# Kernel optimization log

Measured on AMD Instinct MI355X. Metric: run time of the kernel, lower is better.

The kernel has to match this reference:

```python
import jax, jax.numpy as jnp
import numpy as np

B, D_IN, H, D_OUT = 256, 512, 512, 10
S = 32          # num posterior samples
MAXITER = 10    # fixed CG steps (solve_normaleq_cg_fixed_step_reortho(maxiter=10))
EPS = 1e-12


def mlp(params, x):
    W1, b1, W2, b2 = params
    h = jnp.tanh(x @ W1 + b1)
    return h @ W2 + b2  # [B, D_OUT]


def setup_inputs() -> dict:
    key = jax.random.key(0)
    ks = jax.random.split(key, 8)
    s = lambda k, shape, scale=1.0: jax.random.normal(k, shape, dtype=jnp.float32) * scale
    return {
        "x": s(ks[0], (B, D_IN)),
        "W1": s(ks[1], (D_IN, H), 1.0 / np.sqrt(D_IN)),
        "b1": jnp.zeros((H,), jnp.float32),
        "W2": s(ks[2], (H, D_OUT), 1.0 / np.sqrt(H)),
        "b2": jnp.zeros((D_OUT,), jnp.float32),
        "eps_W1": s(ks[3], (S, D_IN, H)),
        "eps_b1": s(ks[4], (S, H)),
        "eps_W2": s(ks[5], (S, H, D_OUT)),
        "eps_b2": s(ks[6], (S, D_OUT)),
        "log_precision": jnp.zeros((), jnp.float32),
        "log_scale_image": jnp.asarray(-2.0, jnp.float32),
    }


def _posterior_predict(x, W1, b1, W2, b2, eps_W1, eps_b1, eps_W2, eps_b2,
                       log_precision, log_scale_image):
    params = (W1, b1, W2, b2)
    f = lambda p: mlp(p, x)
    out0, jvp_lin = jax.linearize(f, params)  # out0: [B, D_OUT]
    _, vjp_fn = jax.vjp(f, params)
    N = B * D_OUT

    def matvec(u_flat):  # u: [N] -> (J J^T) u : [N]
        (t,) = vjp_fn(u_flat.reshape(B, D_OUT))  # J^T u (param pytree)
        return jvp_lin(t).ravel()                # J J^T u

    def cg_reortho(b):  # fixed-step CG with full reorthogonalization
        rn0 = jnp.linalg.norm(b)
        basis0 = jnp.zeros((MAXITER + 1, N), b.dtype).at[0].set(b / (rn0 + EPS))

        def step(carry, k):
            a, r, p, basis = carry
            Ap = matvec(p)
            rr = jnp.vdot(r, r)
            alpha = rr / (jnp.vdot(p, Ap) + EPS)
            a = a + alpha * p
            r_new = r - alpha * Ap
            # Gram-Schmidt reorthogonalization against stored residual basis
            r_new = r_new - basis.T @ (basis @ r_new)
            beta = jnp.vdot(r_new, r_new) / (rr + EPS)
            p = r_new + beta * p
            basis = basis.at[k + 1].set(r_new / (jnp.linalg.norm(r_new) + EPS))
            return (a, r_new, p, basis), jnp.linalg.norm(r_new)

        init = (jnp.zeros_like(b), b, b, basis0)
        (a, _, _, _), resnorms = jax.lax.scan(step, init, jnp.arange(MAXITER))
        return a, resnorms

    def kernel_projection(eps):  # eps: param-pytree iso noise sample
        b = jvp_lin(eps).ravel()          # J v
        a, resnorms = cg_reortho(b)       # (J J^T)^{-1} J v
        (kv,) = vjp_fn(a.reshape(B, D_OUT))  # kernel component J^T a
        return kv, resnorms

    iso = (eps_W1, eps_b1, eps_W2, eps_b2)  # leading axis S
    kernel, resnorms = jax.vmap(kernel_projection)(iso)
    image = jax.tree_util.tree_map(lambda i, k: i - k, iso, kernel)

    # linearized output sampling: f(mean) + J @ (s_k * kernel + s_i * image)
    sk = jnp.exp(-0.5 * log_precision)  # log_scale_kernel = -0.5 * log_precision
    si = jnp.exp(log_scale_image)
    perturb = jax.tree_util.tree_map(lambda kv, iv: sk * kv + si * iv, kernel, image)
    preds = out0[None] + jax.vmap(jvp_lin)(perturb)  # [S, B, D_OUT]
    return preds


def reference(x, W1, b1, W2, b2, eps_W1, eps_b1, eps_W2, eps_b2,
              log_precision, log_scale_image):
    return _posterior_predict(x, W1, b1, W2, b2, eps_W1, eps_b1, eps_W2,
                              eps_b2, log_precision, log_scale_image)
```

## Files before the change

kernel.cpp:

```cpp
#include <hip/hip_runtime.h>
#include <math.h>

#define BB    256
#define DIN   512
#define HD    512
#define DOUT  10
#define NS    32
#define NIDX  2560
#define MAXIT 10
#define CG_EPS 1e-12f

typedef __attribute__((ext_vector_type(8))) short s16x8;
typedef __attribute__((ext_vector_type(4))) float f32x4;

__device__ __forceinline__ float wave_red(float v){
  #pragma unroll
  for (int off = 32; off > 0; off >>= 1) v += __shfl_down(v, off, 64);
  return v;
}
__device__ __forceinline__ unsigned short f2bf(float f){
  unsigned u = __float_as_uint(f);
  return (unsigned short)((u + 0x7FFFu + ((u >> 16) & 1u)) >> 16);
}
__device__ __forceinline__ float bf2f(unsigned short h){
  return __uint_as_float((unsigned)h << 16);
}

__global__ __launch_bounds__(256) void k_gemm_z(
    const float* __restrict__ x, const float* __restrict__ W1,
    const float* __restrict__ b1, float* __restrict__ h, float* __restrict__ G)
{
  __shared__ __align__(16) float Al[16][68];
  __shared__ __align__(16) float Bl[16][64];
  const int tid = threadIdx.x;
  const int m0 = blockIdx.y * 64, n0 = blockIdx.x * 64;
  const int tx = tid & 15, ty = tid >> 4;
  float acc[4][4] = {};
  for (int k0 = 0; k0 < DIN; k0 += 16){
    {
      int m = tid >> 2, kk = (tid & 3) << 2;
      float4 a = *(const float4*)(x + (size_t)(m0+m)*DIN + k0 + kk);
      Al[kk+0][m]=a.x; Al[kk+1][m]=a.y; Al[kk+2][m]=a.z; Al[kk+3][m]=a.w;
    }
    {
      int kk = tid >> 4, n = (tid & 15) << 2;
      *(float4*)&Bl[kk][n] = *(const float4*)(W1 + (size_t)(k0+kk)*HD + n0 + n);
    }
    __syncthreads();
    #pragma unroll
    for (int kk = 0; kk < 16; kk++){
      float4 av = *(const float4*)&Al[kk][ty<<2];
      float4 bv = *(const float4*)&Bl[kk][tx<<2];
      float aa[4]={av.x,av.y,av.z,av.w}, bb[4]={bv.x,bv.y,bv.z,bv.w};
      #pragma unroll
      for (int i=0;i<4;i++)
        #pragma unroll
        for (int j=0;j<4;j++) acc[i][j] += aa[i]*bb[j];
    }
    __syncthreads();
  }
  float4 b4 = *(const float4*)&b1[n0 + (tx<<2)];
  float bbv[4] = {b4.x,b4.y,b4.z,b4.w};
  #pragma unroll
  for (int i=0;i<4;i++){
    int m = m0 + (ty<<2) + i;
    float hh[4], gg[4];
    #pragma unroll
    for (int j=0;j<4;j++){ float t = tanhf(acc[i][j] + bbv[j]); hh[j]=t; gg[j]=1.0f-t*t; }
    *(float4*)&h[(size_t)m*HD + n0 + (tx<<2)] = make_float4(hh[0],hh[1],hh[2],hh[3]);
    *(float4*)&G[(size_t)m*HD + n0 + (tx<<2)] = make_float4(gg[0],gg[1],gg[2],gg[3]);
  }
}

__global__ __launch_bounds__(256) void k_gemm_kxkh(
    const float* __restrict__ x, const float* __restrict__ h,
    float* __restrict__ Kx, float* __restrict__ Kh)
{
  __shared__ __align__(16) float Al[16][68];
  __shared__ __align__(16) float Bl[16][68];
  const int tid = threadIdx.x;
  const float* A = blockIdx.z ? h : x;
  float* C = blockIdx.z ? Kh : Kx;
  const int m0 = blockIdx.y * 64, n0 = blockIdx.x * 64;
  const int tx = tid & 15, ty = tid >> 4;
  float acc[4][4] = {};
  for (int k0 = 0; k0 < DIN; k0 += 16){
    {
      int m = tid >> 2, kk = (tid & 3) << 2;
      float4 a = *(const float4*)(A + (size_t)(m0+m)*DIN + k0 + kk);
      Al[kk+0][m]=a.x; Al[kk+1][m]=a.y; Al[kk+2][m]=a.z; Al[kk+3][m]=a.w;
      float4 b = *(const float4*)(A + (size_t)(n0+m)*DIN + k0 + kk);
      Bl[kk+0][m]=b.x; Bl[kk+1][m]=b.y; Bl[kk+2][m]=b.z; Bl[kk+3][m]=b.w;
    }
    __syncthreads();
    #pragma unroll
    for (int kk = 0; kk < 16; kk++){
      float4 av = *(const float4*)&Al[kk][ty<<2];
      float4 bv = *(const float4*)&Bl[kk][tx<<2];
      float aa[4]={av.x,av.y,av.z,av.w}, bb[4]={bv.x,bv.y,bv.z,bv.w};
      #pragma unroll
      for (int i=0;i<4;i++)
        #pragma unroll
        for (int j=0;j<4;j++) acc[i][j] += aa[i]*bb[j];
    }
    __syncthreads();
  }
  #pragma unroll
  for (int i=0;i<4;i++){
    int m = m0 + (ty<<2) + i;
    *(float4*)&C[(size_t)m*BB + n0 + (tx<<2)] =
        make_float4(acc[i][0]+1.0f, acc[i][1]+1.0f, acc[i][2]+1.0f, acc[i][3]+1.0f);
  }
}

__global__ __launch_bounds__(256) void k_buildE(
    const float* __restrict__ G, const float* __restrict__ W2,
    unsigned short* __restrict__ E2)
{
  int gid = blockIdx.x * 256 + threadIdx.x;
  int row = gid >> 7, j4 = (gid & 127) << 2;
  int b = row / 10, o = row - b * 10;
  float4 g = *(const float4*)&G[(size_t)b*HD + j4];
  float e[4] = { g.x * W2[(j4+0)*DOUT + o], g.y * W2[(j4+1)*DOUT + o],
                 g.z * W2[(j4+2)*DOUT + o], g.w * W2[(j4+3)*DOUT + o] };
  unsigned short hi[4], lo[4];
  #pragma unroll
  for (int r = 0; r < 4; r++){
    hi[r] = f2bf(e[r]);
    lo[r] = f2bf(e[r] - bf2f(hi[r]));
  }
  *(ushort4*)&E2[(size_t)row*1024 + j4]       = make_ushort4(hi[0],hi[1],hi[2],hi[3]);
  *(ushort4*)&E2[(size_t)row*1024 + 512 + j4] = make_ushort4(lo[0],lo[1],lo[2],lo[3]);
}

__global__ __launch_bounds__(256) void k_prepx(
    const float* __restrict__ x, unsigned short* __restrict__ x2)
{
  int gid = blockIdx.x * 256 + threadIdx.x;
  int row = gid >> 7, j4 = (gid & 127) << 2;
  float4 v = *(const float4*)&x[(size_t)row*DIN + j4];
  float e[4] = {v.x, v.y, v.z, v.w};
  unsigned short hi[4], lo[4];
  #pragma unroll
  for (int r = 0; r < 4; r++){
    hi[r] = f2bf(e[r]);
    lo[r] = f2bf(e[r] - bf2f(hi[r]));
  }
  *(ushort4*)&x2[(size_t)row*1024 + j4]       = make_ushort4(hi[0],hi[1],hi[2],hi[3]);
  *(ushort4*)&x2[(size_t)row*1024 + 512 + j4] = make_ushort4(lo[0],lo[1],lo[2],lo[3]);
}

__global__ __launch_bounds__(128) void k_gemm_M(
    const unsigned short* __restrict__ E2, const float* __restrict__ Kx,
    const float* __restrict__ Kh, unsigned short* __restrict__ M2)
{
  __shared__ float red[64][66];
  const int tid = threadIdx.x;
  const int w = tid >> 6, l = tid & 63;
  const int bi = blockIdx.y, bj = blockIdx.x;
  const int m0 = bi << 6, n0 = bj << 6;
  const int ln = l & 15, kq = l >> 4;

  const unsigned short* pa[4];
  const unsigned short* pb[4];
  #pragma unroll
  for (int f = 0; f < 4; f++){
    pa[f] = E2 + (size_t)(m0 + f*16 + ln) * 1024 + kq * 8;
    pb[f] = E2 + (size_t)(n0 + f*16 + ln) * 1024 + kq * 8;
  }

  f32x4 acc[4][4];
  #pragma unroll
  for (int i = 0; i < 4; i++)
    #pragma unroll
    for (int j = 0; j < 4; j++)
      acc[i][j] = (f32x4){0.f, 0.f, 0.f, 0.f};

  s16x8 a0[4], b0[4], a1[4], b1[4];

#define LOAD_AB(Aset, Bset, s) do{                                        \
    const int _ph = (s) >> 4, _kk = ((s) & 15) << 5;                      \
    const int _oa = (_ph == 2 ? 512 : 0) + _kk;                           \
    const int _ob = (_ph == 1 ? 512 : 0) + _kk;                           \
    Aset[0] = *(const s16x8*)(pa[0] + _oa);                               \
    Aset[1] = *(const s16x8*)(pa[1] + _oa);                               \
    Aset[2] = *(const s16x8*)(pa[2] + _oa);                               \
    Aset[3] = *(const s16x8*)(pa[3] + _oa);                               \
    Bset[0] = *(const s16x8*)(pb[0] + _ob);                               \
    Bset[1] = *(const s16x8*)(pb[1] + _ob);                               \
    Bset[2] = *(const s16x8*)(pb[2] + _ob);                               \
    Bset[3] = *(const s16x8*)(pb[3] + _ob);                               \
  }while(0)

#define MFMA_AB(Aset, Bset) do{                                           \
    _Pragma("unroll")                                                     \
    for (int fi = 0; fi < 4; fi++){                                       \
      _Pragma("unroll")                                                   \
      for (int fj = 0; fj < 4; fj++)                                      \
        acc[fi][fj] = __builtin_amdgcn_mfma_f32_16x16x32_bf16(            \
            Aset[fi], Bset[fj], acc[fi][fj], 0, 0, 0);                    \
    }                                                                     \
  }while(0)

  const int sbase = 24 * w;
  LOAD_AB(a0, b0, sbase);
  for (int it = 0; it < 12; ++it){
    LOAD_AB(a1, b1, sbase + 2*it + 1);
    MFMA_AB(a0, b0);
    if (it < 11) LOAD_AB(a0, b0, sbase + 2*it + 2);
    MFMA_AB(a1, b1);
  }
#undef LOAD_AB
#undef MFMA_AB

  if (w == 1){
    #pragma unroll
    for (int fi = 0; fi < 4; fi++)
      #pragma unroll
      for (int fj = 0; fj < 4; fj++)
        #pragma unroll
        for (int q = 0; q < 4; q++)
          red[16*fi + kq*4 + q][16*fj + ln] = acc[fi][fj][q];
  }
  __syncthreads();
  if (w == 0){
    #pragma unroll
    for (int fi = 0; fi < 4; fi++)
      #pragma unroll
      for (int fj = 0; fj < 4; fj++)
        #pragma unroll
        for (int q = 0; q < 4; q++)
          acc[fi][fj][q] += red[16*fi + kq*4 + q][16*fj + ln];

    int bmv[4][4], omv[4][4], bnv[4], onv[4];
    #pragma unroll
    for (int f = 0; f < 4; f++){
      int n = n0 + f*16 + ln; bnv[f] = n / 10; onv[f] = n - bnv[f]*10;
      #pragma unroll
      for (int r = 0; r < 4; r++){
        int m = m0 + f*16 + kq*4 + r;
        bmv[f][r] = m / 10; omv[f][r] = m - bmv[f][r]*10;
      }
    }
    #pragma unroll
    for (int fi = 0; fi < 4; fi++)
      #pragma unroll
      for (int r = 0; r < 4; r++){
        const int m = m0 + fi*16 + kq*4 + r;
        #pragma unroll
        for (int fj = 0; fj < 4; fj++){
          const int n = n0 + fj*16 + ln;
          float v = Kx[(size_t)bmv[fi][r]*BB + bnv[fj]] * acc[fi][fj][r];
          if (omv[fi][r] == onv[fj]) v += Kh[(size_t)bmv[fi][r]*BB + bnv[fj]];
          unsigned short hv = f2bf(v);
          M2[(size_t)m*5120 + n]        = hv;
          M2[(size_t)m*5120 + 2560 + n] = f2bf(v - bf2f(hv));
        }
      }
  }
}

__global__ __launch_bounds__(512) void k_gemm_T(
    const unsigned short* __restrict__ x2, const float* __restrict__ eW1,
    const float* __restrict__ eb1, const float* __restrict__ G,
    float* __restrict__ T)
{
  const int tid = threadIdx.x;
  const int w = tid >> 6, l = tid & 63;
  const int ln = l & 15, kq = l >> 4;
  const int n0 = blockIdx.x << 6;
  const int s  = blockIdx.y;
  const float* Wb = eW1 + (size_t)s * DIN * HD;

  const unsigned short* pa[2];
  #pragma unroll
  for (int f = 0; f < 2; f++)
    pa[f] = x2 + (size_t)(16*(2*w + f) + ln) * 1024 + kq * 8;

  f32x4 acc[2][4];
  #pragma unroll
  for (int i = 0; i < 2; i++)
    #pragma unroll
    for (int j = 0; j < 4; j++)
      acc[i][j] = (f32x4){0.f, 0.f, 0.f, 0.f};

  #pragma unroll 2
  for (int k0 = 0; k0 < DIN; k0 += 32){
    float wv[4][8];
    const float* wp = Wb + (size_t)(k0 + kq*8)*HD + n0 + ln;
    #pragma unroll
    for (int i = 0; i < 8; i++)
      #pragma unroll
      for (int f = 0; f < 4; f++)
        wv[f][i] = wp[(size_t)i*HD + 16*f];

    s16x8 ahi[2], alo[2], bhi[4], blo[4];
    #pragma unroll
    for (int f = 0; f < 2; f++){
      ahi[f] = *(const s16x8*)(pa[f] + k0);
      alo[f] = *(const s16x8*)(pa[f] + 512 + k0);
    }
    #pragma unroll
    for (int f = 0; f < 4; f++)
      #pragma unroll
      for (int i = 0; i < 8; i++){
        unsigned short hh = f2bf(wv[f][i]);
        bhi[f][i] = (short)hh;
        blo[f][i] = (short)f2bf(wv[f][i] - bf2f(hh));
      }
    #pragma unroll
    for (int fi = 0; fi < 2; fi++)
      #pragma unroll
      for (int fj = 0; fj < 4; fj++){
        acc[fi][fj] = __builtin_amdgcn_mfma_f32_16x16x32_bf16(ahi[fi], bhi[fj], acc[fi][fj], 0,0,0);
        acc[fi][fj] = __builtin_amdgcn_mfma_f32_16x16x32_bf16(ahi[fi], blo[fj], acc[fi][fj], 0,0,0);
        acc[fi][fj] = __builtin_amdgcn_mfma_f32_16x16x32_bf16(alo[fi], bhi[fj], acc[fi][fj], 0,0,0);
      }
  }

  #pragma unroll
  for (int fj = 0; fj < 4; fj++){
    const int n = n0 + 16*fj + ln;
    const float eb = eb1[(size_t)s*HD + n];
    #pragma unroll
    for (int fi = 0; fi < 2; fi++)
      #pragma unroll
      for (int q = 0; q < 4; q++){
        const int m = 16*(2*w + fi) + kq*4 + q;
        T[((size_t)s*BB + m)*HD + n] = (acc[fi][fj][q] + eb) * G[(size_t)m*HD + n];
      }
  }
}

__global__ __launch_bounds__(256) void k_bvec(
    const float* __restrict__ T, const float* __restrict__ W2,
    const float* __restrict__ h, const float* __restrict__ eW2,
    const float* __restrict__ eb2, const float* __restrict__ b2,
    float* __restrict__ bvec, float* __restrict__ out0, float* __restrict__ rr0_part)
{
  __shared__ __align__(16) float W2t[10][516];
  __shared__ __align__(16) float E2t[10][516];
  __shared__ float wl[4];
  const int tid = threadIdx.x, bid = blockIdx.x;
  const int s = bid / 10;
  const int idx = (bid % 10) * 256 + tid;
  const int b = idx / 10, o = idx - b*10;
  const float* e2 = eW2 + (size_t)s * HD * DOUT;
  for (int i = tid; i < HD*DOUT; i += 256){
    int k = i / 10, oo = i - k*10;
    W2t[oo][k] = W2[i];
    E2t[oo][k] = e2[i];
  }
  __syncthreads();
  const float* Tr = T + ((size_t)s*BB + b) * HD;
  const float* hr = h + (size_t)b * HD;
  const bool do0 = (bid < 10);
  float acc = eb2[s*DOUT + o];
  float a0 = 0.f;
  #pragma unroll 4
  for (int k4 = 0; k4 < HD/4; k4++){
    float4 t4 = *(const float4*)(Tr + (k4<<2));
    float4 h4 = *(const float4*)(hr + (k4<<2));
    float4 w4 = *(const float4*)&W2t[o][k4<<2];
    float4 q4 = *(const float4*)&E2t[o][k4<<2];
    acc += t4.x*w4.x + t4.y*w4.y + t4.z*w4.z + t4.w*w4.w
         + h4.x*q4.x + h4.y*q4.y + h4.z*q4.z + h4.w*q4.w;
    if (do0) a0 += h4.x*w4.x + h4.y*w4.y + h4.z*w4.z + h4.w*w4.w;
  }
  bvec[(size_t)s*NIDX + idx] = acc;
  if (do0) out0[idx] = a0 + b2[o];
  float v = wave_red(acc * acc);
  if ((tid & 63) == 0) wl[tid >> 6] = v;
  __syncthreads();
  if (tid == 0) rr0_part[bid] = wl[0]+wl[1]+wl[2]+wl[3];
}

__global__ __launch_bounds__(256) void k_init(
    const float* __restrict__ bvec, const float* __restrict__ rr0_part,
    float* __restrict__ r, float* __restrict__ p, float* __restrict__ a,
    float* __restrict__ basis, float* __restrict__ rr_arr,
    unsigned short* __restrict__ ps2)
{
  int gid = blockIdx.x * 256 + threadIdx.x;
  int s = gid / NIDX, idx = gid - s * NIDX;
  float rr0 = 0.f;
  #pragma unroll
  for (int i = 0; i < 10; i++) rr0 += rr0_part[s*10 + i];
  float bv = bvec[gid];
  r[gid] = bv; p[gid] = bv; a[gid] = 0.f;
  basis[gid] = bv / (sqrtf(rr0) + CG_EPS);
  unsigned short hh = f2bf(bv);
  ps2[(size_t)s*5120 + idx]        = hh;
  ps2[(size_t)s*5120 + 2560 + idx] = f2bf(bv - bf2f(hh));
  if (threadIdx.x == 0) rr_arr[s] = rr0;
}

__global__ __launch_bounds__(256) void k_matvec(
    const unsigned short* __restrict__ M2, const unsigned short* __restrict__ p2,
    float* __restrict__ Ap_part)
{
  __shared__ float red[4][32][33];
  const int tid = threadIdx.x;
  const int w = tid >> 6, l = tid & 63;
  const int ln = l & 15, kq = l >> 4;
  const int R0 = blockIdx.x << 5;
  const int kh = blockIdx.y;
  const int c0 = kh*1280 + w*320;

  const unsigned short* a0p = M2 + (size_t)(R0 + ln)*5120      + c0 + kq*8;
  const unsigned short* a1p = M2 + (size_t)(R0 + 16 + ln)*5120 + c0 + kq*8;
  const unsigned short* q0  = p2 + (size_t)ln*5120             + c0 + kq*8;
  const unsigned short* q1  = p2 + (size_t)(16 + ln)*5120      + c0 + kq*8;

  f32x4 acc[2][2];
  #pragma unroll
  for (int i = 0; i < 2; i++)
    #pragma unroll
    for (int j = 0; j < 2; j++) acc[i][j] = (f32x4){0.f,0.f,0.f,0.f};

  #pragma unroll 2
  for (int ch = 0; ch < 10; ch++){
    const int o = ch * 32;
    s16x8 bh0 = *(const s16x8*)(q0 + o);
    s16x8 bl0 = *(const s16x8*)(q0 + 2560 + o);
    s16x8 bh1 = *(const s16x8*)(q1 + o);
    s16x8 bl1 = *(const s16x8*)(q1 + 2560 + o);
    s16x8 a0h = *(const s16x8*)(a0p + o);
    s16x8 a0l = *(const s16x8*)(a0p + 2560 + o);
    s16x8 a1h = *(const s16x8*)(a1p + o);
    s16x8 a1l = *(const s16x8*)(a1p + 2560 + o);
    acc[0][0] = __builtin_amdgcn_mfma_f32_16x16x32_bf16(a0h, bh0, acc[0][0], 0,0,0);
    acc[0][1] = __builtin_amdgcn_mfma_f32_16x16x32_bf16(a0h, bh1, acc[0][1], 0,0,0);
    acc[1][0] = __builtin_amdgcn_mfma_f32_16x16x32_bf16(a1h, bh0, acc[1][0], 0,0,0);
    acc[1][1] = __builtin_amdgcn_mfma_f32_16x16x32_bf16(a1h, bh1, acc[1][1], 0,0,0);
    acc[0][0] = __builtin_amdgcn_mfma_f32_16x16x32_bf16(a0h, bl0, acc[0][0], 0,0,0);
    acc[0][1] = __builtin_amdgcn_mfma_f32_16x16x32_bf16(a0h, bl1, acc[0][1], 0,0,0);
    acc[1][0] = __builtin_amdgcn_mfma_f32_16x16x32_bf16(a1h, bl0, acc[1][0], 0,0,0);
    acc[1][1] = __builtin_amdgcn_mfma_f32_16x16x32_bf16(a1h, bl1, acc[1][1], 0,0,0);
    acc[0][0] = __builtin_amdgcn_mfma_f32_16x16x32_bf16(a0l, bh0, acc[0][0], 0,0,0);
    acc[0][1] = __builtin_amdgcn_mfma_f32_16x16x32_bf16(a0l, bh1, acc[0][1], 0,0,0);
    acc[1][0] = __builtin_amdgcn_mfma_f32_16x16x32_bf16(a1l, bh0, acc[1][0], 0,0,0);
    acc[1][1] = __builtin_amdgcn_mfma_f32_16x16x32_bf16(a1l, bh1, acc[1][1], 0,0,0);
  }

  #pragma unroll
  for (int f = 0; f < 2; f++)
    #pragma unroll
    for (int g = 0; g < 2; g++)
      #pragma unroll
      for (int q = 0; q < 4; q++)
        red[w][16*f + kq*4 + q][16*g + ln] = acc[f][g][q];
  __syncthreads();
  #pragma unroll
  for (int j = 0; j < 4; j++){
    const int idx = tid + (j << 8);
    const int r = idx & 31, s = idx >> 5;
    float v = red[0][r][s] + red[1][r][s] + red[2][r][s] + red[3][r][s];
    Ap_part[((size_t)kh*NS + s)*NIDX + R0 + r] = v;
  }
}

__global__ __launch_bounds__(256) void k_cg(
    const float* __restrict__ Ap_part, float* __restrict__ rr_arr, int k, int last,
    float* __restrict__ pv, unsigned short* __restrict__ ps2,
    unsigned short* __restrict__ as2,
    float* __restrict__ av, float* __restrict__ rv, float* __restrict__ basis)
{
  __shared__ float wl[4];
  __shared__ float red[4][10];
  __shared__ float cbr[10];
  const int s = blockIdx.x, tid = threadIdx.x;
  const size_t base = (size_t)s * NIDX;
  const float rr = rr_arr[s];

  float ap[10], pvv[10];
  #pragma unroll
  for (int c = 0; c < 10; c++){
    const int idx = tid + (c << 8);
    ap[c]  = Ap_part[base + idx] + Ap_part[(size_t)NS*NIDX + base + idx];
    pvv[c] = pv[base + idx];
  }
  float v = 0.f;
  #pragma unroll
  for (int c = 0; c < 10; c++) v += pvv[c] * ap[c];
  v = wave_red(v);
  if ((tid & 63) == 0) wl[tid >> 6] = v;
  __syncthreads();
  const float pAp = wl[0]+wl[1]+wl[2]+wl[3];
  const float alpha = rr / (pAp + CG_EPS);

  float rn[10];
  #pragma unroll
  for (int c = 0; c < 10; c++){
    const int idx = tid + (c << 8);
    const float an = av[base + idx] + alpha * pvv[c];
    av[base + idx] = an;
    rn[c] = rv[base + idx] - alpha * ap[c];
    if (last){
      unsigned short hh = f2bf(an);
      as2[(size_t)s*5120 + idx]        = hh;
      as2[(size_t)s*5120 + 2560 + idx] = f2bf(an - bf2f(hh));
    }
  }

  for (int j = 0; j <= k; j++){
    float cv = 0.f;
    const float* brow = basis + (size_t)j * (NS*NIDX) + base;
    #pragma unroll
    for (int c = 0; c < 10; c++) cv += brow[tid + (c << 8)] * rn[c];
    cv = wave_red(cv);
    if ((tid & 63) == 0) red[tid >> 6][j] = cv;
  }
  __syncthreads();
  if (tid <= k) cbr[tid] = red[0][tid]+red[1][tid]+red[2][tid]+red[3][tid];
  __syncthreads();

  for (int j = 0; j <= k; j++){
    const float cc = cbr[j];
    const float* brow = basis + (size_t)j * (NS*NIDX) + base;
    #pragma unroll
    for (int c = 0; c < 10; c++) rn[c] -= brow[tid + (c << 8)] * cc;
  }

  float rr2 = 0.f;
  #pragma unroll
  for (int c = 0; c < 10; c++) rr2 += rn[c]*rn[c];
  rr2 = wave_red(rr2);
  __syncthreads();
  if ((tid & 63) == 0) wl[tid >> 6] = rr2;
  __syncthreads();
  const float rrn = wl[0]+wl[1]+wl[2]+wl[3];
  const float beta = rrn / (rr + CG_EPS);
  const float inv  = 1.0f / (sqrtf(rrn) + CG_EPS);

  float* bnew = basis + (size_t)(k+1) * (NS*NIDX) + base;
  #pragma unroll
  for (int c = 0; c < 10; c++){
    const int idx = tid + (c << 8);
    const float pnew = rn[c] + beta * pvv[c];
    rv[base + idx] = rn[c];
    pv[base + idx] = pnew;
    bnew[idx] = rn[c] * inv;
    unsigned short hh = f2bf(pnew);
    ps2[(size_t)s*5120 + idx]        = hh;
    ps2[(size_t)s*5120 + 2560 + idx] = f2bf(pnew - bf2f(hh));
  }
  if (tid == 0) rr_arr[s] = rrn;
}

__global__ __launch_bounds__(256) void k_final(
    const float* __restrict__ out0, const float* __restrict__ bvec,
    const float* __restrict__ Ap_part, const float* __restrict__ lp,
    const float* __restrict__ lsi, float* __restrict__ out)
{
  int gid = blockIdx.x * 256 + threadIdx.x;
  int s = gid / NIDX, idx = gid - s * NIDX;
  float sk = expf(-0.5f * lp[0]);
  float si = expf(lsi[0]);
  float ma = Ap_part[gid] + Ap_part[(size_t)NS*NIDX + gid];
  out[gid] = out0[idx] + si * bvec[gid] + (sk - si) * ma;
}

extern "C" void kernel_launch(void* const* d_in, const int* in_sizes, int n_in,
                              void* d_out, int out_size, void* d_ws, size_t ws_size,
                              hipStream_t stream)
{
  const float* x   = (const float*)d_in[0];
  const float* W1  = (const float*)d_in[1];
  const float* b1  = (const float*)d_in[2];
  const float* W2  = (const float*)d_in[3];
  const float* b2  = (const float*)d_in[4];
  const float* eW1 = (const float*)d_in[5];
  const float* eb1 = (const float*)d_in[6];
  const float* eW2 = (const float*)d_in[7];
  const float* eb2 = (const float*)d_in[8];
  const float* lp  = (const float*)d_in[9];
  const float* lsi = (const float*)d_in[10];
  float* outp = (float*)d_out;

  float* ws = (float*)d_ws;
  float* h        = ws;
  float* G        = h        + 131072;
  float* Kx       = G        + 131072;
  float* Kh       = Kx       + 65536;
  float* E2f      = Kh       + 65536;
  float* x2f      = E2f      + 1310720;
  float* M2f      = x2f      + 131072;
  float* out0     = M2f      + 6553600;
  float* bvec     = out0     + 2560;
  float* rv       = bvec     + 81920;
  float* pv       = rv       + 81920;
  float* av       = pv       + 81920;
  float* basis    = av       + 81920;
  float* Ap_part  = basis    + 901120;
  float* ps2f     = Ap_part  + 163840;
  float* as2f     = ps2f     + 81920;
  float* rr0_part = as2f     + 81920;
  float* rr_arr   = rr0_part + 320;

  unsigned short* E2  = (unsigned short*)E2f;
  unsigned short* x2  = (unsigned short*)x2f;
  unsigned short* M2  = (unsigned short*)M2f;
  unsigned short* ps2 = (unsigned short*)ps2f;
  unsigned short* as2 = (unsigned short*)as2f;
  float* T = M2f;

  k_gemm_z   <<<dim3(8,4),   256, 0, stream>>>(x, W1, b1, h, G);
  k_buildE   <<<1280,        256, 0, stream>>>(G, W2, E2);
  k_prepx    <<<128,         256, 0, stream>>>(x, x2);
  k_gemm_kxkh<<<dim3(4,4,2), 256, 0, stream>>>(x, h, Kx, Kh);
  k_gemm_T   <<<dim3(8,32),  512, 0, stream>>>(x2, eW1, eb1, G, T);
  k_bvec     <<<320,         256, 0, stream>>>(T, W2, h, eW2, eb2, b2, bvec, out0, rr0_part);
  k_gemm_M   <<<dim3(40,40), 128, 0, stream>>>(E2, Kx, Kh, M2);
  k_init     <<<320,         256, 0, stream>>>(bvec, rr0_part, rv, pv, av, basis, rr_arr, ps2);

  for (int k = 0; k < MAXIT; k++){
    k_matvec<<<dim3(80,2), 256, 0, stream>>>(M2, ps2, Ap_part);
    k_cg    <<<NS,         256, 0, stream>>>(Ap_part, rr_arr, k, (k == MAXIT-1),
                                             pv, ps2, as2, av, rv, basis);
  }

  k_matvec<<<dim3(80,2), 256, 0, stream>>>(M2, as2, Ap_part);
  k_final <<<320,        256, 0, stream>>>(out0, bvec, Ap_part, lp, lsi, outp);
}
```

Before: 450.0 us.

## Stage k_gemm_M tiles in LDS via direct loads; split matvec K four ways

k_gemm_M no longer has each wave load its own operands from global memory and then reduce a split-K through LDS. Instead a 128x64 block loads swizzled tiles into LDS with global_load_lds and both waves reuse the shared B tile, which removes the cross-wave reduction. The matvec's K dimension is split into four partitions instead of two to get more blocks, and the CG and final kernels now sum four partial buffers. This trades extra partial-sum traffic and more __syncthreads for better operand reuse and parallelism.

```diff
diff --git a/kernel.cpp b/kernel.cpp
--- a/kernel.cpp
+++ b/kernel.cpp
@@ -24,6 +24,12 @@
 }
 __device__ __forceinline__ float bf2f(unsigned short h){
   return __uint_as_float((unsigned)h << 16);
+}
+
+typedef const __attribute__((address_space(1))) unsigned short gus_t;
+typedef __attribute__((address_space(3))) unsigned short lus_t;
+__device__ __forceinline__ void gload16(const unsigned short* g, unsigned short* l){
+  __builtin_amdgcn_global_load_lds((gus_t*)g, (lus_t*)l, 16, 0, 0);
 }
 
 __global__ __launch_bounds__(256) void k_gemm_z(
@@ -154,20 +160,19 @@
     const unsigned short* __restrict__ E2, const float* __restrict__ Kx,
     const float* __restrict__ Kh, unsigned short* __restrict__ M2)
 {
-  __shared__ float red[64][66];
+  __shared__ __align__(16) unsigned short As[128*64];
+  __shared__ __align__(16) unsigned short Bs[64*64];
   const int tid = threadIdx.x;
   const int w = tid >> 6, l = tid & 63;
-  const int bi = blockIdx.y, bj = blockIdx.x;
-  const int m0 = bi << 6, n0 = bj << 6;
   const int ln = l & 15, kq = l >> 4;
-
-  const unsigned short* pa[4];
-  const unsigned short* pb[4];
-  #pragma unroll
-  for (int f = 0; f < 4; f++){
-    pa[f] = E2 + (size_t)(m0 + f*16 + ln) * 1024 + kq * 8;
-    pb[f] = E2 + (size_t)(n0 + f*16 + ln) * 1024 + kq * 8;
-  }
+  const int m0 = blockIdx.y << 7, n0 = blockIdx.x << 6;
+
+  const int srow = tid >> 3;
+  const int scc  = (tid & 7) ^ (srow & 7);
+  const unsigned short* gA = E2 + (size_t)(m0 + srow)*1024 + scc*8;
+  const unsigned short* gB = E2 + (size_t)(n0 + srow)*1024 + scc*8;
+  unsigned short* lA = As + ((tid & 64) << 3);
+  unsigned short* lB = Bs + ((tid & 64) << 3);
 
   f32x4 acc[4][4];
   #pragma unroll
@@ -176,88 +181,66 @@
     for (int j = 0; j < 4; j++)
       acc[i][j] = (f32x4){0.f, 0.f, 0.f, 0.f};
 
-  s16x8 a0[4], b0[4], a1[4], b1[4];
-
-#define LOAD_AB(Aset, Bset, s) do{                                        \
-    const int _ph = (s) >> 4, _kk = ((s) & 15) << 5;                      \
-    const int _oa = (_ph == 2 ? 512 : 0) + _kk;                           \
-    const int _ob = (_ph == 1 ? 512 : 0) + _kk;                           \
-    Aset[0] = *(const s16x8*)(pa[0] + _oa);                               \
-    Aset[1] = *(const s16x8*)(pa[1] + _oa);                               \
-    Aset[2] = *(const s16x8*)(pa[2] + _oa);                               \
-    Aset[3] = *(const s16x8*)(pa[3] + _oa);                               \
-    Bset[0] = *(const s16x8*)(pb[0] + _ob);                               \
-    Bset[1] = *(const s16x8*)(pb[1] + _ob);                               \
-    Bset[2] = *(const s16x8*)(pb[2] + _ob);                               \
-    Bset[3] = *(const s16x8*)(pb[3] + _ob);                               \
-  }while(0)
-
-#define MFMA_AB(Aset, Bset) do{                                           \
-    _Pragma("unroll")                                                     \
-    for (int fi = 0; fi < 4; fi++){                                       \
-      _Pragma("unroll")                                                   \
-      for (int fj = 0; fj < 4; fj++)                                      \
-        acc[fi][fj] = __builtin_amdgcn_mfma_f32_16x16x32_bf16(            \
-            Aset[fi], Bset[fj], acc[fi][fj], 0, 0, 0);                    \
-    }                                                                     \
-  }while(0)
-
-  const int sbase = 24 * w;
-  LOAD_AB(a0, b0, sbase);
-  for (int it = 0; it < 12; ++it){
-    LOAD_AB(a1, b1, sbase + 2*it + 1);
-    MFMA_AB(a0, b0);
-    if (it < 11) LOAD_AB(a0, b0, sbase + 2*it + 2);
-    MFMA_AB(a1, b1);
-  }
-#undef LOAD_AB
-#undef MFMA_AB
-
-  if (w == 1){
-    #pragma unroll
-    for (int fi = 0; fi < 4; fi++)
-      #pragma unroll
-      for (int fj = 0; fj < 4; fj++)
+  const int xs = ln & 7;
+
+  for (int t = 0; t < 24; ++t){
+    const int p = t >> 3, k8 = t & 7;
+    const int oa = ((p == 2) ? 512 : 0) + (k8 << 6);
+    const int ob = ((p == 1) ? 512 : 0) + (k8 << 6);
+    #pragma unroll
+    for (int c = 0; c < 8; c++)
+      gload16(gA + (size_t)c*16*1024 + oa, lA + c*1024);
+    #pragma unroll
+    for (int c = 0; c < 4; c++)
+      gload16(gB + (size_t)c*16*1024 + ob, lB + c*1024);
+    __syncthreads();
+
+    #pragma unroll
+    for (int kk = 0; kk < 2; kk++){
+      const int kc = kq + (kk << 2);
+      const int co = (kc ^ xs) << 3;
+      s16x8 af[4], bf[4];
+      #pragma unroll
+      for (int f = 0; f < 4; f++){
+        af[f] = *(const s16x8*)(As + ((w<<6) + (f<<4) + ln)*64 + co);
+        bf[f] = *(const s16x8*)(Bs + ((f<<4) + ln)*64 + co);
+      }
+      #pragma unroll
+      for (int fi = 0; fi < 4; fi++)
         #pragma unroll
-        for (int q = 0; q < 4; q++)
-          red[16*fi + kq*4 + q][16*fj + ln] = acc[fi][fj][q];
-  }
-  __syncthreads();
-  if (w == 0){
-    #pragma unroll
-    for (int fi = 0; fi < 4; fi++)
-      #pragma unroll
-      for (int fj = 0; fj < 4; fj++)
-        #pragma unroll
-        for (int q = 0; q < 4; q++)
-          acc[fi][fj][q] += red[16*fi + kq*4 + q][16*fj + ln];
-
-    int bmv[4][4], omv[4][4], bnv[4], onv[4];
-    #pragma unroll
-    for (int f = 0; f < 4; f++){
-      int n = n0 + f*16 + ln; bnv[f] = n / 10; onv[f] = n - bnv[f]*10;
-      #pragma unroll
-      for (int r = 0; r < 4; r++){
-        int m = m0 + f*16 + kq*4 + r;
-        bmv[f][r] = m / 10; omv[f][r] = m - bmv[f][r]*10;
+        for (int fj = 0; fj < 4; fj++)
+          acc[fi][fj] = __builtin_amdgcn_mfma_f32_16x16x32_bf16(
+              af[fi], bf[fj], acc[fi][fj], 0, 0, 0);
+    }
+    __syncthreads();
+  }
+
+  const int mb = m0 + (w << 6);
+  int bmv[4][4], omv[4][4], bnv[4], onv[4];
+  #pragma unroll
+  for (int f = 0; f < 4; f++){
+    int n = n0 + f*16 + ln; bnv[f] = n / 10; onv[f] = n - bnv[f]*10;
+    #pragma unroll
+    for (int r = 0; r < 4; r++){
+      int m = mb + f*16 + kq*4 + r;
+      bmv[f][r] = m / 10; omv[f][r] = m - bmv[f][r]*10;
+    }
+  }
+  #pragma unroll
+  for (int fi = 0; fi < 4; fi++)
+    #pragma unroll
+    for (int r = 0; r < 4; r++){
+      const int m = mb + fi*16 + kq*4 + r;
+      #pragma unroll
+      for (int fj = 0; fj < 4; fj++){
+        const int n = n0 + fj*16 + ln;
+        float v = Kx[(size_t)bmv[fi][r]*BB + bnv[fj]] * acc[fi][fj][r];
+        if (omv[fi][r] == onv[fj]) v += Kh[(size_t)bmv[fi][r]*BB + bnv[fj]];
+        unsigned short hv = f2bf(v);
+        M2[(size_t)m*5120 + n]        = hv;
+        M2[(size_t)m*5120 + 2560 + n] = f2bf(v - bf2f(hv));
       }
     }
-    #pragma unroll
-    for (int fi = 0; fi < 4; fi++)
-      #pragma unroll
-      for (int r = 0; r < 4; r++){
-        const int m = m0 + fi*16 + kq*4 + r;
-        #pragma unroll
-        for (int fj = 0; fj < 4; fj++){
-          const int n = n0 + fj*16 + ln;
-          float v = Kx[(size_t)bmv[fi][r]*BB + bnv[fj]] * acc[fi][fj][r];
-          if (omv[fi][r] == onv[fj]) v += Kh[(size_t)bmv[fi][r]*BB + bnv[fj]];
-          unsigned short hv = f2bf(v);
-          M2[(size_t)m*5120 + n]        = hv;
-          M2[(size_t)m*5120 + 2560 + n] = f2bf(v - bf2f(hv));
-        }
-      }
-  }
 }
 
 __global__ __launch_bounds__(512) void k_gemm_T(
@@ -405,7 +388,7 @@
   const int ln = l & 15, kq = l >> 4;
   const int R0 = blockIdx.x << 5;
   const int kh = blockIdx.y;
-  const int c0 = kh*1280 + w*320;
+  const int c0 = kh*640 + w*160;
 
   const unsigned short* a0p = M2 + (size_t)(R0 + ln)*5120      + c0 + kq*8;
   const unsigned short* a1p = M2 + (size_t)(R0 + 16 + ln)*5120 + c0 + kq*8;
@@ -418,8 +401,8 @@
     #pragma unroll
     for (int j = 0; j < 2; j++) acc[i][j] = (f32x4){0.f,0.f,0.f,0.f};
 
-  #pragma unroll 2
-  for (int ch = 0; ch < 10; ch++){
+  #pragma unroll
+  for (int ch = 0; ch < 5; ch++){
     const int o = ch * 32;
     s16x8 bh0 = *(const s16x8*)(q0 + o);
     s16x8 bl0 = *(const s16x8*)(q0 + 2560 + o);
@@ -477,7 +460,11 @@
   #pragma unroll
   for (int c = 0; c < 10; c++){
     const int idx = tid + (c << 8);
-    ap[c]  = Ap_part[base + idx] + Ap_part[(size_t)NS*NIDX + base + idx];
+    float apv = 0.f;
+    #pragma unroll
+    for (int kc = 0; kc < 4; kc++)
+      apv += Ap_part[((size_t)kc*NS + s)*NIDX + idx];
+    ap[c]  = apv;
     pvv[c] = pv[base + idx];
   }
   float v = 0.f;
@@ -557,7 +544,9 @@
   int s = gid / NIDX, idx = gid - s * NIDX;
   float sk = expf(-0.5f * lp[0]);
   float si = expf(lsi[0]);
-  float ma = Ap_part[gid] + Ap_part[(size_t)NS*NIDX + gid];
+  float ma = 0.f;
+  #pragma unroll
+  for (int kc = 0; kc < 4; kc++) ma += Ap_part[(size_t)kc*NS*NIDX + gid];
   out[gid] = out0[idx] + si * bvec[gid] + (sk - si) * ma;
 }
 
@@ -593,7 +582,7 @@
   float* av       = pv       + 81920;
   float* basis    = av       + 81920;
   float* Ap_part  = basis    + 901120;
-  float* ps2f     = Ap_part  + 163840;
+  float* ps2f     = Ap_part  + 327680;
   float* as2f     = ps2f     + 81920;
   float* rr0_part = as2f     + 81920;
   float* rr_arr   = rr0_part + 320;
@@ -611,15 +600,15 @@
   k_gemm_kxkh<<<dim3(4,4,2), 256, 0, stream>>>(x, h, Kx, Kh);
   k_gemm_T   <<<dim3(8,32),  512, 0, stream>>>(x2, eW1, eb1, G, T);
   k_bvec     <<<320,         256, 0, stream>>>(T, W2, h, eW2, eb2, b2, bvec, out0, rr0_part);
-  k_gemm_M   <<<dim3(40,40), 128, 0, stream>>>(E2, Kx, Kh, M2);
+  k_gemm_M   <<<dim3(40,20), 128, 0, stream>>>(E2, Kx, Kh, M2);
   k_init     <<<320,         256, 0, stream>>>(bvec, rr0_part, rv, pv, av, basis, rr_arr, ps2);
 
   for (int k = 0; k < MAXIT; k++){
-    k_matvec<<<dim3(80,2), 256, 0, stream>>>(M2, ps2, Ap_part);
+    k_matvec<<<dim3(80,4), 256, 0, stream>>>(M2, ps2, Ap_part);
     k_cg    <<<NS,         256, 0, stream>>>(Ap_part, rr_arr, k, (k == MAXIT-1),
                                              pv, ps2, as2, av, rv, basis);
   }
 
-  k_matvec<<<dim3(80,2), 256, 0, stream>>>(M2, as2, Ap_part);
+  k_matvec<<<dim3(80,4), 256, 0, stream>>>(M2, as2, Ap_part);
   k_final <<<320,        256, 0, stream>>>(out0, bvec, Ap_part, lp, lsi, outp);
 }
```

Result: faster. 397.3 us (median of 4 runs) (-11.7%).
